# Kernel tuning notes

Measured on AMD Instinct MI355X. Metric: run time of the kernel, lower is better.

Reference implementation:

```python
import jax, jax.numpy as jnp
import numpy as np

NUM_GROUPS = 32
NUM_HEADS = 8
EPS = 1e-5


def setup_inputs() -> dict:
    key = jax.random.key(0)
    ks = jax.random.split(key, 4)
    b, c, h, w = 16, 512, 32, 32
    x = jax.random.normal(ks[0], (b, c, h, w), dtype=jnp.float32)
    norm_w = jnp.ones((c,), dtype=jnp.float32)
    norm_b = jnp.zeros((c,), dtype=jnp.float32)
    qkv_w = jax.random.normal(ks[1], (3 * c, c), dtype=jnp.float32) * (1.0 / np.sqrt(c))
    qkv_b = jnp.zeros((3 * c,), dtype=jnp.float32)
    proj_w = jax.random.normal(ks[2], (c, c), dtype=jnp.float32) * (1.0 / np.sqrt(c))
    proj_b = jnp.zeros((c,), dtype=jnp.float32)
    return {"x": x, "norm_w": norm_w, "norm_b": norm_b,
            "qkv_w": qkv_w, "qkv_b": qkv_b, "proj_w": proj_w, "proj_b": proj_b}


def group_norm(x, weight, bias):
    b, c, h, w = x.shape
    xg = x.reshape(b, NUM_GROUPS, c // NUM_GROUPS, h * w)
    mean = xg.mean(axis=(2, 3), keepdims=True)
    var = xg.var(axis=(2, 3), keepdims=True)
    xn = (xg - mean) * jax.lax.rsqrt(var + EPS)
    xn = xn.reshape(b, c, h, w)
    return xn * weight[None, :, None, None] + bias[None, :, None, None]


def reference(x, norm_w, norm_b, qkv_w, qkv_b, proj_w, proj_b):
    b, c, h, w = x.shape
    n = h * w
    head = NUM_HEADS
    ch = c // head

    x_norm = group_norm(x, norm_w, norm_b)
    # 1x1 conv == channel matmul: [b,3c,n]
    xf = x_norm.reshape(b, c, n)
    qkv = jnp.einsum('oc,bcn->bon', qkv_w, xf) + qkv_b[None, :, None]
    q, k, v = jnp.split(qkv, 3, axis=1)  # each [b,c,n]
    q = q.reshape(b, head, ch, n) * (ch ** -0.5)
    k = k.reshape(b, head, ch, n)
    v = v.reshape(b, head, ch, n)

    attn = jnp.einsum('bhcn,bhcm->bhnm', q, k)
    attn = jax.nn.softmax(attn, axis=-1)
    out = jnp.einsum('bhnm,bhcm->bhcn', attn, v)  # [b,head,ch,n]
    out = out.reshape(b, c, n)
    out = jnp.einsum('oc,bcn->bon', proj_w, out) + proj_b[None, :, None]
    return x + out.reshape(b, c, h, w)
```

## Files before the change

kernel.cpp:

```cpp
#include <hip/hip_runtime.h>

typedef short short8 __attribute__((ext_vector_type(8)));
typedef float f32x4 __attribute__((ext_vector_type(4)));

#define B_   16
#define C_   512
#define N_   1024
#define NH_  8
#define CH_  64
#define G_   32
#define CPG_ 16

__device__ inline float b2f(unsigned int u) {
    union { unsigned int i; float f; } v; v.i = u << 16; return v.f;
}
__device__ inline unsigned short f2b(float f) {
    union { float f; unsigned int i; } v; v.f = f;
    unsigned int r = v.i + 0x7fffu + ((v.i >> 16) & 1u);
    return (unsigned short)(r >> 16);
}
__device__ inline unsigned int pack2(float a, float b) {
    return (unsigned int)f2b(a) | ((unsigned int)f2b(b) << 16);
}
__device__ inline unsigned int asu(float f) {
    union { float f; unsigned int i; } v; v.f = f; return v.i;
}
__device__ inline unsigned int packtr(float a, float b) {
    return __builtin_amdgcn_perm(asu(b), asu(a), 0x07060302u);
}
__device__ inline void gload16(const void* g, void* l) {
    __builtin_amdgcn_global_load_lds(
        (const __attribute__((address_space(1))) void*)g,
        (__attribute__((address_space(3))) void*)l, 16, 0, 0);
}

__global__ __launch_bounds__(256) void gnconv_kernel(const float* __restrict__ x,
                                                     const float* __restrict__ nw,
                                                     const float* __restrict__ nb,
                                                     unsigned short* __restrict__ xnT,
                                                     const float* __restrict__ qkvw,
                                                     const float* __restrict__ projw,
                                                     unsigned short* __restrict__ wq,
                                                     unsigned short* __restrict__ wp)
{
    __shared__ float red[8];
    int t = threadIdx.x;

    if (blockIdx.x >= 512) {
        const int NQ = 3 * C_ * C_;
        int idx = (((int)blockIdx.x - 512) * 256 + t) * 8;
        const float* src; unsigned short* dst; int j;
        if (idx < NQ) { src = qkvw;  dst = wq; j = idx; }
        else          { src = projw; dst = wp; j = idx - NQ; }
        float4 u0 = *(const float4*)(src + j);
        float4 u1 = *(const float4*)(src + j + 4);
        uint4 p;
        p.x = pack2(u0.x, u0.y); p.y = pack2(u0.z, u0.w);
        p.z = pack2(u1.x, u1.y); p.w = pack2(u1.z, u1.w);
        *(uint4*)(dst + j) = p;
        return;
    }

    int b = blockIdx.x >> 5, g = blockIdx.x & 31;
    const float* base = x + ((size_t)(b * C_ + g * CPG_)) * N_;

    float s = 0.f, ss = 0.f;
    for (int it = 0; it < 16; ++it) {
        int idx = (it * 256 + t) * 4;
        float4 u = *(const float4*)(base + idx);
        s  += u.x + u.y + u.z + u.w;
        ss += u.x * u.x + u.y * u.y + u.z * u.z + u.w * u.w;
    }
#pragma unroll
    for (int off = 1; off < 64; off <<= 1) {
        s  += __shfl_xor(s, off);
        ss += __shfl_xor(ss, off);
    }
    int wv = t >> 6;
    if ((t & 63) == 0) { red[wv * 2] = s; red[wv * 2 + 1] = ss; }
    __syncthreads();
    s  = red[0] + red[2] + red[4] + red[6];
    ss = red[1] + red[3] + red[5] + red[7];
    float mean = s * (1.f / 16384.f);
    float var  = ss * (1.f / 16384.f) - mean * mean;
    float rstd = rsqrtf(var + 1e-5f);

    float sc[16], sh[16];
#pragma unroll
    for (int ch = 0; ch < 16; ++ch) {
        float wv_ = nw[g * CPG_ + ch];
        float bv_ = nb[g * CPG_ + ch];
        sc[ch] = wv_ * rstd;
        sh[ch] = bv_ - mean * sc[ch];
    }

#pragma unroll
    for (int nbi = 0; nbi < 2; ++nbi) {
        int n = nbi * 512 + t * 2;
        float2 v[16];
#pragma unroll
        for (int ch = 0; ch < 16; ++ch)
            v[ch] = *(const float2*)(base + (size_t)ch * N_ + n);
#pragma unroll
        for (int col = 0; col < 2; ++col) {
            float f[16];
#pragma unroll
            for (int ch = 0; ch < 16; ++ch) {
                float xv = col ? v[ch].y : v[ch].x;
                f[ch] = xv * sc[ch] + sh[ch];
            }
            uint4 o0, o1;
            o0.x = pack2(f[0], f[1]);  o0.y = pack2(f[2], f[3]);
            o0.z = pack2(f[4], f[5]);  o0.w = pack2(f[6], f[7]);
            o1.x = pack2(f[8], f[9]);  o1.y = pack2(f[10], f[11]);
            o1.z = pack2(f[12], f[13]); o1.w = pack2(f[14], f[15]);
            unsigned short* dst = xnT + ((size_t)(b * N_ + n + col)) * C_ + g * CPG_;
            *(uint4*)dst = o0;
            *(uint4*)(dst + 8) = o1;
        }
    }
}

__global__ __launch_bounds__(256) void qkv_kernel(const unsigned short* __restrict__ w,
                                                  const float* __restrict__ bias,
                                                  const unsigned short* __restrict__ xnT,
                                                  unsigned short* __restrict__ qT,
                                                  unsigned short* __restrict__ kT,
                                                  unsigned short* __restrict__ vv)
{
    __shared__ unsigned short Als[128 * 64], Bls[128 * 64];
    int t = threadIdx.x;
    int n0 = blockIdx.x * 128, m0 = blockIdx.y * 128, b = blockIdx.z;
    int lane = t & 63, wv = t >> 6;
    int l = lane & 15, qd = lane >> 4;
    int wm = (wv >> 1) * 64, wn = (wv & 1) * 64;
    f32x4 acc[4][4] = {};
    const unsigned short* Bbase = xnT + ((size_t)(b * N_ + n0)) * C_;

    int grow = lane >> 3, gcol = ((lane & 7) ^ grow) * 8;
    const unsigned short* pA[4]; const unsigned short* pB[4];
    unsigned short* lA[4]; unsigned short* lB[4];
#pragma unroll
    for (int g = 0; g < 4; ++g) {
        int r = wv * 32 + g * 8 + grow;
        pA[g] = w + (size_t)(m0 + r) * C_ + gcol;
        pB[g] = Bbase + (size_t)r * C_ + gcol;
        lA[g] = &Als[(wv * 32 + g * 8) * 64];
        lB[g] = &Bls[(wv * 32 + g * 8) * 64];
    }

    for (int kk = 0; kk < 8; ++kk) {
        int ko = kk * 64;
#pragma unroll
        for (int g = 0; g < 4; ++g) {
            gload16(pA[g] + ko, lA[g]);
            gload16(pB[g] + ko, lB[g]);
        }
        __builtin_amdgcn_s_waitcnt(0);
        __syncthreads();
#pragma unroll
        for (int ks = 0; ks < 2; ++ks) {
            short8 aF[4], bF[4];
#pragma unroll
            for (int i = 0; i < 4; ++i) {
                int ra = wm + i * 16 + l;
                aF[i] = *(const short8*)&Als[ra * 64 + (((ks * 4 + qd) ^ (l & 7)) * 8)];
                int rb = wn + i * 16 + l;
                bF[i] = *(const short8*)&Bls[rb * 64 + (((ks * 4 + qd) ^ (l & 7)) * 8)];
            }
#pragma unroll
            for (int mt = 0; mt < 4; ++mt)
#pragma unroll
                for (int nt = 0; nt < 4; ++nt)
                    acc[mt][nt] = __builtin_amdgcn_mfma_f32_16x16x32_bf16(aF[mt], bF[nt], acc[mt][nt], 0, 0, 0);
        }
        __syncthreads();
    }

    int o_base = m0 + wm;
    int sec = o_base >> 9;
    int oc = o_base & 511;
    int h = oc >> 6;
    float bv[4][4];
#pragma unroll
    for (int mt = 0; mt < 4; ++mt)
#pragma unroll
        for (int r = 0; r < 4; ++r)
            bv[mt][r] = bias[o_base + mt * 16 + qd * 4 + r];

    if (sec < 2) {
        unsigned short* dst = (sec == 0) ? qT : kT;
        float scl = (sec == 0) ? (0.125f * 1.44269504f) : 1.0f;
#pragma unroll
        for (int mt = 0; mt < 4; ++mt)
#pragma unroll
            for (int nt = 0; nt < 4; ++nt) {
                int n = n0 + wn + nt * 16 + l;
                ushort4 o;
                o.x = f2b((acc[mt][nt][0] + bv[mt][0]) * scl);
                o.y = f2b((acc[mt][nt][1] + bv[mt][1]) * scl);
                o.z = f2b((acc[mt][nt][2] + bv[mt][2]) * scl);
                o.w = f2b((acc[mt][nt][3] + bv[mt][3]) * scl);
                *(ushort4*)(dst + ((size_t)(b * NH_ + h) * N_ + n) * CH_ + mt * 16 + qd * 4) = o;
            }
    } else {
#pragma unroll
        for (int mt = 0; mt < 4; ++mt)
#pragma unroll
            for (int nt = 0; nt < 4; ++nt) {
                int n = n0 + wn + nt * 16 + l;
#pragma unroll
                for (int r = 0; r < 4; ++r) {
                    int ch = mt * 16 + qd * 4 + r;
                    vv[((size_t)(b * NH_ + h) * CH_ + ch) * N_ + n] = f2b(acc[mt][nt][r] + bv[mt][r]);
                }
            }
    }
}

__global__ __launch_bounds__(256, 4) void attn_kernel(const unsigned short* __restrict__ qT,
                                                      const unsigned short* __restrict__ kT,
                                                      const unsigned short* __restrict__ vv,
                                                      unsigned short* __restrict__ at)
{
    __shared__ unsigned short Ks[2][4096];
    __shared__ unsigned short Vs[2][4096];

    int t = threadIdx.x, lane = t & 63, wv = t >> 6;
    int l = lane & 15, qd = lane >> 4;
    int blk = blockIdx.x;
    int ibk = blk >> 7;
    int bh  = blk & 127;
    int h = bh & 7, b = bh >> 3;
    int i0 = ibk * 128 + wv * 32;
    const size_t hoff = (size_t)bh * (size_t)N_ * CH_;
    const unsigned short* qbase = qT + hoff;
    const unsigned short* kbase = kT + hoff;
    const unsigned short* vbase = vv + hoff;

    int plok;
    {
        unsigned int ta = (unsigned int)lane, tb = 64u + (unsigned int)lane;
        asm volatile("v_permlane32_swap_b32 %0, %1" : "+v"(ta), "+v"(tb));
        asm volatile("v_permlane16_swap_b32 %0, %1" : "+v"(ta), "+v"(tb));
        unsigned int e1 = (unsigned int)((lane >> 4) * 32 + (lane & 15));
        plok = __all(ta == e1) && __all(tb == e1 + 16u);
    }

    short8 qF[2][2];
#pragma unroll
    for (int it = 0; it < 2; ++it)
#pragma unroll
        for (int ks = 0; ks < 2; ++ks)
            qF[it][ks] = *(const short8*)(qbase + (size_t)(i0 + it * 16 + l) * CH_ + ks * 32 + qd * 8);

    int srow = t >> 2, sc16 = (t & 3) * 16;
    int sw = srow & 7, bb = (t & 3) * 2;
    int d0 = srow * 64 + ((bb ^ sw) * 8);
    int d1 = srow * 64 + (((bb + 1) ^ sw) * 8);
    const unsigned short* kSrc = kbase + (size_t)srow * CH_ + sc16;
    const unsigned short* vSrc = vbase + (size_t)srow * N_ + sc16;

    f32x4 Oa[4][2] = {};
    float lsum[2] = {0.f, 0.f};
    int la0 = (qd & 1) * 32 + l;
    int la1 = la0 + 16;
    int swl = l & 7;

    uint4 ku0, ku1, vu0, vu1;
    {
        const uint4* kp = (const uint4*)(kSrc);
        ku0 = kp[0]; ku1 = kp[1];
        const uint4* vp2 = (const uint4*)(vSrc);
        vu0 = vp2[0]; vu1 = vp2[1];
        *(uint4*)&Ks[0][d0] = ku0; *(uint4*)&Ks[0][d1] = ku1;
        *(uint4*)&Vs[0][d0] = vu0; *(uint4*)&Vs[0][d1] = vu1;
        kp  = (const uint4*)(kSrc + 4096);
        ku0 = kp[0]; ku1 = kp[1];
        vp2 = (const uint4*)(vSrc + 64);
        vu0 = vp2[0]; vu1 = vp2[1];
    }

    for (int tile = 0; tile < 16; ++tile) {
        __syncthreads();
        if (tile < 15) {
            unsigned short* Kw = Ks[(tile + 1) & 1];
            unsigned short* Vw = Vs[(tile + 1) & 1];
            *(uint4*)&Kw[d0] = ku0; *(uint4*)&Kw[d1] = ku1;
            *(uint4*)&Vw[d0] = vu0; *(uint4*)&Vw[d1] = vu1;
            if (tile < 14) {
                const uint4* kp = (const uint4*)(kSrc + (size_t)(tile + 2) * 4096);
                ku0 = kp[0]; ku1 = kp[1];
                const uint4* vp2 = (const uint4*)(vSrc + (size_t)(tile + 2) * 64);
                vu0 = vp2[0]; vu1 = vp2[1];
            }
        }
        const unsigned short* Kb = Ks[tile & 1];
        const unsigned short* Vb = Vs[tile & 1];

        short8 kA[2][2][2];
#pragma unroll
        for (int jb = 0; jb < 2; ++jb)
#pragma unroll
            for (int jt = 0; jt < 2; ++jt)
#pragma unroll
                for (int ks = 0; ks < 2; ++ks)
                    kA[jb][jt][ks] = *(const short8*)&Kb[(jb * 32 + jt * 16 + l) * 64 + (((ks * 4 + qd) ^ swl) * 8)];
        f32x4 Sa[2][2][2] = {};
#pragma unroll
        for (int jb = 0; jb < 2; ++jb)
#pragma unroll
            for (int jt = 0; jt < 2; ++jt)
#pragma unroll
                for (int it = 0; it < 2; ++it)
#pragma unroll
                    for (int ks = 0; ks < 2; ++ks)
                        Sa[jb][jt][it] = __builtin_amdgcn_mfma_f32_16x16x32_bf16(kA[jb][jt][ks], qF[it][ks], Sa[jb][jt][it], 0, 0, 0);

        unsigned int pk[2][2][2][2];
        float ls0 = 0.f, ls1 = 0.f;
#pragma unroll
        for (int jb = 0; jb < 2; ++jb)
#pragma unroll
            for (int jt = 0; jt < 2; ++jt)
#pragma unroll
                for (int it = 0; it < 2; ++it) {
                    float p0 = __builtin_amdgcn_exp2f(Sa[jb][jt][it][0]);
                    float p1 = __builtin_amdgcn_exp2f(Sa[jb][jt][it][1]);
                    float p2 = __builtin_amdgcn_exp2f(Sa[jb][jt][it][2]);
                    float p3 = __builtin_amdgcn_exp2f(Sa[jb][jt][it][3]);
                    float q01 = (p0 + p1) + (p2 + p3);
                    if (it == 0) ls0 += q01; else ls1 += q01;
                    pk[jb][jt][it][0] = packtr(p0, p1);
                    pk[jb][jt][it][1] = packtr(p2, p3);
                }
        lsum[0] += ls0; lsum[1] += ls1;

        short8 bP[2][2];
        if (plok) {
#pragma unroll
            for (int jb = 0; jb < 2; ++jb)
#pragma unroll
                for (int it = 0; it < 2; ++it) {
                    union { short8 s; unsigned int u[4]; } fb;
                    unsigned int a0 = pk[jb][0][it][0], c0 = pk[jb][1][it][0];
                    asm volatile("v_permlane32_swap_b32 %0, %1" : "+v"(a0), "+v"(c0));
                    asm volatile("v_permlane16_swap_b32 %0, %1" : "+v"(a0), "+v"(c0));
                    unsigned int a1 = pk[jb][0][it][1], c1 = pk[jb][1][it][1];
                    asm volatile("v_permlane32_swap_b32 %0, %1" : "+v"(a1), "+v"(c1));
                    asm volatile("v_permlane16_swap_b32 %0, %1" : "+v"(a1), "+v"(c1));
                    fb.u[0] = a0; fb.u[1] = a1; fb.u[2] = c0; fb.u[3] = c1;
                    bP[jb][it] = fb.s;
                }
        } else {
#pragma unroll
            for (int jb = 0; jb < 2; ++jb)
#pragma unroll
                for (int it = 0; it < 2; ++it) {
                    union { short8 s; unsigned int u[4]; } fb;
                    unsigned int a0 = (unsigned int)__shfl((int)pk[jb][0][it][0], la0);
                    unsigned int b0 = (unsigned int)__shfl((int)pk[jb][1][it][0], la0);
                    fb.u[0] = (qd < 2) ? a0 : b0;
                    unsigned int a1 = (unsigned int)__shfl((int)pk[jb][0][it][1], la0);
                    unsigned int b1 = (unsigned int)__shfl((int)pk[jb][1][it][1], la0);
                    fb.u[1] = (qd < 2) ? a1 : b1;
                    unsigned int a2 = (unsigned int)__shfl((int)pk[jb][0][it][0], la1);
                    unsigned int b2 = (unsigned int)__shfl((int)pk[jb][1][it][0], la1);
                    fb.u[2] = (qd < 2) ? a2 : b2;
                    unsigned int a3 = (unsigned int)__shfl((int)pk[jb][0][it][1], la1);
                    unsigned int b3 = (unsigned int)__shfl((int)pk[jb][1][it][1], la1);
                    fb.u[3] = (qd < 2) ? a3 : b3;
                    bP[jb][it] = fb.s;
                }
        }

#pragma unroll
        for (int jb = 0; jb < 2; ++jb) {
            short8 vA[4];
#pragma unroll
            for (int cht = 0; cht < 4; ++cht)
                vA[cht] = *(const short8*)&Vb[(cht * 16 + l) * 64 + (((jb * 4 + qd) ^ swl) * 8)];
#pragma unroll
            for (int cht = 0; cht < 4; ++cht)
#pragma unroll
                for (int it = 0; it < 2; ++it)
                    Oa[cht][it] = __builtin_amdgcn_mfma_f32_16x16x32_bf16(vA[cht], bP[jb][it], Oa[cht][it], 0, 0, 0);
        }
    }

#pragma unroll
    for (int it = 0; it < 2; ++it) {
        float lt = lsum[it];
        lt += __shfl_xor(lt, 16);
        lt += __shfl_xor(lt, 32);
        float inv = 1.0f / lt;
        int i = i0 + it * 16 + l;
        unsigned short* dst = at + ((size_t)(b * N_ + i)) * C_ + h * CH_;
#pragma unroll
        for (int cht = 0; cht < 4; ++cht) {
            ushort4 o;
            o.x = f2b(Oa[cht][it][0] * inv);
            o.y = f2b(Oa[cht][it][1] * inv);
            o.z = f2b(Oa[cht][it][2] * inv);
            o.w = f2b(Oa[cht][it][3] * inv);
            *(ushort4*)(dst + cht * 16 + qd * 4) = o;
        }
    }
}

__global__ __launch_bounds__(256) void proj_kernel(const unsigned short* __restrict__ w,
                                                   const float* __restrict__ bias,
                                                   const unsigned short* __restrict__ at,
                                                   const float* __restrict__ x,
                                                   float* __restrict__ out)
{
    __shared__ unsigned short Als[128 * 64], Bls[128 * 64];
    int t = threadIdx.x;
    int n0 = blockIdx.x * 128, m0 = blockIdx.y * 128, b = blockIdx.z;
    int lane = t & 63, wv = t >> 6;
    int l = lane & 15, qd = lane >> 4;
    int wm = (wv >> 1) * 64, wn = (wv & 1) * 64;
    f32x4 acc[4][4] = {};
    const unsigned short* Bbase = at + ((size_t)(b * N_ + n0)) * C_;

    int grow = lane >> 3, gcol = ((lane & 7) ^ grow) * 8;
    const unsigned short* pA[4]; const unsigned short* pB[4];
    unsigned short* lA[4]; unsigned short* lB[4];
#pragma unroll
    for (int g = 0; g < 4; ++g) {
        int r = wv * 32 + g * 8 + grow;
        pA[g] = w + (size_t)(m0 + r) * C_ + gcol;
        pB[g] = Bbase + (size_t)r * C_ + gcol;
        lA[g] = &Als[(wv * 32 + g * 8) * 64];
        lB[g] = &Bls[(wv * 32 + g * 8) * 64];
    }

    for (int kk = 0; kk < 8; ++kk) {
        int ko = kk * 64;
#pragma unroll
        for (int g = 0; g < 4; ++g) {
            gload16(pA[g] + ko, lA[g]);
            gload16(pB[g] + ko, lB[g]);
        }
        __builtin_amdgcn_s_waitcnt(0);
        __syncthreads();
#pragma unroll
        for (int ks = 0; ks < 2; ++ks) {
            short8 aF[4], bF[4];
#pragma unroll
            for (int i = 0; i < 4; ++i) {
                int ra = wm + i * 16 + l;
                aF[i] = *(const short8*)&Als[ra * 64 + (((ks * 4 + qd) ^ (l & 7)) * 8)];
                int rb = wn + i * 16 + l;
                bF[i] = *(const short8*)&Bls[rb * 64 + (((ks * 4 + qd) ^ (l & 7)) * 8)];
            }
#pragma unroll
            for (int mt = 0; mt < 4; ++mt)
#pragma unroll
                for (int nt = 0; nt < 4; ++nt)
                    acc[mt][nt] = __builtin_amdgcn_mfma_f32_16x16x32_bf16(aF[mt], bF[nt], acc[mt][nt], 0, 0, 0);
        }
        __syncthreads();
    }

    float bv[4][4];
#pragma unroll
    for (int mt = 0; mt < 4; ++mt)
#pragma unroll
        for (int r = 0; r < 4; ++r)
            bv[mt][r] = bias[m0 + wm + mt * 16 + qd * 4 + r];

#pragma unroll
    for (int mt = 0; mt < 4; ++mt)
#pragma unroll
        for (int nt = 0; nt < 4; ++nt) {
            int n = n0 + wn + nt * 16 + l;
#pragma unroll
            for (int r = 0; r < 4; ++r) {
                int o = m0 + wm + mt * 16 + qd * 4 + r;
                size_t idx = ((size_t)b * C_ + o) * N_ + n;
                out[idx] = acc[mt][nt][r] + bv[mt][r] + x[idx];
            }
        }
}

extern "C" void kernel_launch(void* const* d_in, const int* in_sizes, int n_in,
                              void* d_out, int out_size, void* d_ws, size_t ws_size,
                              hipStream_t stream) {
    const float* x     = (const float*)d_in[0];
    const float* nw    = (const float*)d_in[1];
    const float* nb    = (const float*)d_in[2];
    const float* qkvw  = (const float*)d_in[3];
    const float* qkvb  = (const float*)d_in[4];
    const float* projw = (const float*)d_in[5];
    const float* projb = (const float*)d_in[6];
    float* out = (float*)d_out;
    char* ws = (char*)d_ws;
    const size_t SZ = (size_t)B_ * N_ * C_ * 2;
    unsigned short* xnT = (unsigned short*)(ws);
    unsigned short* qTp = (unsigned short*)(ws + SZ);
    unsigned short* kTp = (unsigned short*)(ws + 2 * SZ);
    unsigned short* vp  = (unsigned short*)(ws + 3 * SZ);
    unsigned short* atp = (unsigned short*)(ws);
    unsigned short* wq  = (unsigned short*)(ws + 4 * SZ);
    unsigned short* wp  = (unsigned short*)(ws + 4 * SZ + (size_t)3 * C_ * C_ * 2);

    hipLaunchKernelGGL(gnconv_kernel, dim3(1024), dim3(256), 0, stream, x, nw, nb, xnT, qkvw, projw, wq, wp);
    hipLaunchKernelGGL(qkv_kernel,    dim3(8, 12, B_), dim3(256), 0, stream, wq, qkvb, xnT, qTp, kTp, vp);
    hipLaunchKernelGGL(attn_kernel,   dim3(1024), dim3(256), 0, stream, qTp, kTp, vp, atp);
    hipLaunchKernelGGL(proj_kernel,   dim3(8, 4, B_), dim3(256), 0, stream, wp, projb, atp, x, out);
}
```

Before: 233.6 us.

## Use 16x16x16 bf16 MFMA for PV so P needs no lane permutation

When the 16x16x16 bf16 MFMA builtin exists, the P·V step uses P straight from the QK^T accumulator layout as the A operand. V is read from LDS as 4-element slices instead of 8. This removes the permlane swap and shuffle shuffling of P, and per-jb processing shortens register live ranges. In exchange it issues twice as many smaller MFMAs, and the output store becomes scalar 2-byte writes with extra shuffles for the normalizer.

Result: faster. 219.7 us (-6.0%).

```diff
diff --git a/kernel.cpp b/kernel.cpp
--- a/kernel.cpp
+++ b/kernel.cpp
@@ -1,6 +1,7 @@
 #include <hip/hip_runtime.h>
 
 typedef short short8 __attribute__((ext_vector_type(8)));
+typedef short short4v __attribute__((ext_vector_type(4)));
 typedef float f32x4 __attribute__((ext_vector_type(4)));
 
 #define B_   16
@@ -10,6 +11,10 @@
 #define CH_  64
 #define G_   32
 #define CPG_ 16
+
+#if __has_builtin(__builtin_amdgcn_mfma_f32_16x16x16bf16_1k)
+#define HAVE_M16 1
+#endif
 
 __device__ inline float b2f(unsigned int u) {
     union { unsigned int i; float f; } v; v.i = u << 16; return v.f;
@@ -238,6 +243,7 @@
     const unsigned short* kbase = kT + hoff;
     const unsigned short* vbase = vv + hoff;
 
+#ifndef HAVE_M16
     int plok;
     {
         unsigned int ta = (unsigned int)lane, tb = 64u + (unsigned int)lane;
@@ -246,6 +252,9 @@
         unsigned int e1 = (unsigned int)((lane >> 4) * 32 + (lane & 15));
         plok = __all(ta == e1) && __all(tb == e1 + 16u);
     }
+    int la0 = (qd & 1) * 32 + l;
+    int la1 = la0 + 16;
+#endif
 
     short8 qF[2][2];
 #pragma unroll
@@ -263,8 +272,6 @@
 
     f32x4 Oa[4][2] = {};
     float lsum[2] = {0.f, 0.f};
-    int la0 = (qd & 1) * 32 + l;
-    int la1 = la0 + 16;
     int swl = l & 7;
 
     uint4 ku0, ku1, vu0, vu1;
@@ -297,85 +304,87 @@
         }
         const unsigned short* Kb = Ks[tile & 1];
         const unsigned short* Vb = Vs[tile & 1];
-
-        short8 kA[2][2][2];
-#pragma unroll
-        for (int jb = 0; jb < 2; ++jb)
+#pragma unroll
+        for (int jb = 0; jb < 2; ++jb) {
+            short8 kA[2][2];
 #pragma unroll
             for (int jt = 0; jt < 2; ++jt)
 #pragma unroll
                 for (int ks = 0; ks < 2; ++ks)
-                    kA[jb][jt][ks] = *(const short8*)&Kb[(jb * 32 + jt * 16 + l) * 64 + (((ks * 4 + qd) ^ swl) * 8)];
-        f32x4 Sa[2][2][2] = {};
-#pragma unroll
-        for (int jb = 0; jb < 2; ++jb)
+                    kA[jt][ks] = *(const short8*)&Kb[(jb * 32 + jt * 16 + l) * 64 + (((ks * 4 + qd) ^ swl) * 8)];
+            f32x4 Sa[2][2] = {};
 #pragma unroll
             for (int jt = 0; jt < 2; ++jt)
 #pragma unroll
                 for (int it = 0; it < 2; ++it)
 #pragma unroll
                     for (int ks = 0; ks < 2; ++ks)
-                        Sa[jb][jt][it] = __builtin_amdgcn_mfma_f32_16x16x32_bf16(kA[jb][jt][ks], qF[it][ks], Sa[jb][jt][it], 0, 0, 0);
-
-        unsigned int pk[2][2][2][2];
-        float ls0 = 0.f, ls1 = 0.f;
-#pragma unroll
-        for (int jb = 0; jb < 2; ++jb)
+                        Sa[jt][it] = __builtin_amdgcn_mfma_f32_16x16x32_bf16(kA[jt][ks], qF[it][ks], Sa[jt][it], 0, 0, 0);
+            unsigned int pk[2][2][2];
 #pragma unroll
             for (int jt = 0; jt < 2; ++jt)
 #pragma unroll
                 for (int it = 0; it < 2; ++it) {
-                    float p0 = __builtin_amdgcn_exp2f(Sa[jb][jt][it][0]);
-                    float p1 = __builtin_amdgcn_exp2f(Sa[jb][jt][it][1]);
-                    float p2 = __builtin_amdgcn_exp2f(Sa[jb][jt][it][2]);
-                    float p3 = __builtin_amdgcn_exp2f(Sa[jb][jt][it][3]);
-                    float q01 = (p0 + p1) + (p2 + p3);
-                    if (it == 0) ls0 += q01; else ls1 += q01;
-                    pk[jb][jt][it][0] = packtr(p0, p1);
-                    pk[jb][jt][it][1] = packtr(p2, p3);
+                    float p0 = __builtin_amdgcn_exp2f(Sa[jt][it][0]);
+                    float p1 = __builtin_amdgcn_exp2f(Sa[jt][it][1]);
+                    float p2 = __builtin_amdgcn_exp2f(Sa[jt][it][2]);
+                    float p3 = __builtin_amdgcn_exp2f(Sa[jt][it][3]);
+                    lsum[it] += (p0 + p1) + (p2 + p3);
+                    pk[jt][it][0] = packtr(p0, p1);
+                    pk[jt][it][1] = packtr(p2, p3);
                 }
-        lsum[0] += ls0; lsum[1] += ls1;
-
-        short8 bP[2][2];
-        if (plok) {
-#pragma unroll
-            for (int jb = 0; jb < 2; ++jb)
+#ifdef HAVE_M16
+#pragma unroll
+            for (int jt = 0; jt < 2; ++jt) {
+                short4v bV[4];
+#pragma unroll
+                for (int cht = 0; cht < 4; ++cht) {
+                    int blkv = jb * 4 + jt * 2 + (qd >> 1);
+                    bV[cht] = *(const short4v*)&Vb[(cht * 16 + l) * 64 + ((blkv ^ swl) * 8) + (qd & 1) * 4];
+                }
+#pragma unroll
+                for (int it = 0; it < 2; ++it) {
+                    union { unsigned int u[2]; short4v s; } ap;
+                    ap.u[0] = pk[jt][it][0]; ap.u[1] = pk[jt][it][1];
+#pragma unroll
+                    for (int cht = 0; cht < 4; ++cht)
+                        Oa[cht][it] = __builtin_amdgcn_mfma_f32_16x16x16bf16_1k(ap.s, bV[cht], Oa[cht][it], 0, 0, 0);
+                }
+            }
+#else
+            short8 bP[2];
+            if (plok) {
 #pragma unroll
                 for (int it = 0; it < 2; ++it) {
                     union { short8 s; unsigned int u[4]; } fb;
-                    unsigned int a0 = pk[jb][0][it][0], c0 = pk[jb][1][it][0];
+                    unsigned int a0 = pk[0][it][0], c0 = pk[1][it][0];
                     asm volatile("v_permlane32_swap_b32 %0, %1" : "+v"(a0), "+v"(c0));
                     asm volatile("v_permlane16_swap_b32 %0, %1" : "+v"(a0), "+v"(c0));
-                    unsigned int a1 = pk[jb][0][it][1], c1 = pk[jb][1][it][1];
+                    unsigned int a1 = pk[0][it][1], c1 = pk[1][it][1];
                     asm volatile("v_permlane32_swap_b32 %0, %1" : "+v"(a1), "+v"(c1));
                     asm volatile("v_permlane16_swap_b32 %0, %1" : "+v"(a1), "+v"(c1));
                     fb.u[0] = a0; fb.u[1] = a1; fb.u[2] = c0; fb.u[3] = c1;
-                    bP[jb][it] = fb.s;
+                    bP[it] = fb.s;
                 }
-        } else {
-#pragma unroll
-            for (int jb = 0; jb < 2; ++jb)
+            } else {
 #pragma unroll
                 for (int it = 0; it < 2; ++it) {
                     union { short8 s; unsigned int u[4]; } fb;
-                    unsigned int a0 = (unsigned int)__shfl((int)pk[jb][0][it][0], la0);
-                    unsigned int b0 = (unsigned int)__shfl((int)pk[jb][1][it][0], la0);
+                    unsigned int a0 = (unsigned int)__shfl((int)pk[0][it][0], la0);
+                    unsigned int b0 = (unsigned int)__shfl((int)pk[1][it][0], la0);
                     fb.u[0] = (qd < 2) ? a0 : b0;
-                    unsigned int a1 = (unsigned int)__shfl((int)pk[jb][0][it][1], la0);
-                    unsigned int b1 = (unsigned int)__shfl((int)pk[jb][1][it][1], la0);
+                    unsigned int a1 = (unsigned int)__shfl((int)pk[0][it][1], la0);
+                    unsigned int b1 = (unsigned int)__shfl((int)pk[1][it][1], la0);
                     fb.u[1] = (qd < 2) ? a1 : b1;
-                    unsigned int a2 = (unsigned int)__shfl((int)pk[jb][0][it][0], la1);
-                    unsigned int b2 = (unsigned int)__shfl((int)pk[jb][1][it][0], la1);
+                    unsigned int a2 = (unsigned int)__shfl((int)pk[0][it][0], la1);
+                    unsigned int b2 = (unsigned int)__shfl((int)pk[1][it][0], la1);
                     fb.u[2] = (qd < 2) ? a2 : b2;
-                    unsigned int a3 = (unsigned int)__shfl((int)pk[jb][0][it][1], la1);
-                    unsigned int b3 = (unsigned int)__shfl((int)pk[jb][1][it][1], la1);
+                    unsigned int a3 = (unsigned int)__shfl((int)pk[0][it][1], la1);
+                    unsigned int b3 = (unsigned int)__shfl((int)pk[1][it][1], la1);
                     fb.u[3] = (qd < 2) ? a3 : b3;
-                    bP[jb][it] = fb.s;
+                    bP[it] = fb.s;
                 }
-        }
-
-#pragma unroll
-        for (int jb = 0; jb < 2; ++jb) {
+            }
             short8 vA[4];
 #pragma unroll
             for (int cht = 0; cht < 4; ++cht)
@@ -384,10 +393,30 @@
             for (int cht = 0; cht < 4; ++cht)
 #pragma unroll
                 for (int it = 0; it < 2; ++it)
-                    Oa[cht][it] = __builtin_amdgcn_mfma_f32_16x16x32_bf16(vA[cht], bP[jb][it], Oa[cht][it], 0, 0, 0);
-        }
-    }
-
+                    Oa[cht][it] = __builtin_amdgcn_mfma_f32_16x16x32_bf16(vA[cht], bP[it], Oa[cht][it], 0, 0, 0);
+#endif
+        }
+    }
+
+#ifdef HAVE_M16
+#pragma unroll
+    for (int it = 0; it < 2; ++it) {
+        float lt = lsum[it];
+        lt += __shfl_xor(lt, 16);
+        lt += __shfl_xor(lt, 32);
+        float invv[4];
+#pragma unroll
+        for (int r = 0; r < 4; ++r)
+            invv[r] = 1.0f / __shfl(lt, qd * 4 + r);
+#pragma unroll
+        for (int cht = 0; cht < 4; ++cht)
+#pragma unroll
+            for (int r = 0; r < 4; ++r) {
+                int i = i0 + it * 16 + qd * 4 + r;
+                at[((size_t)(b * N_ + i)) * C_ + h * CH_ + cht * 16 + l] = f2b(Oa[cht][it][r] * invv[r]);
+            }
+    }
+#else
 #pragma unroll
     for (int it = 0; it < 2; ++it) {
         float lt = lsum[it];
@@ -406,6 +435,7 @@
             *(ushort4*)(dst + cht * 16 + qd * 4) = o;
         }
     }
+#endif
 }
 
 __global__ __launch_bounds__(256) void proj_kernel(const unsigned short* __restrict__ w,
```
